# Kernel optimization log

Hardware: AMD Instinct MI355X
Metric: run time of the kernel (lower is better)

## Reference

```python
import jax, jax.numpy as jnp
import numpy as np

NUM_HEADS = 16
FOCUS = 3.0
EPS = 1e-6


def setup_inputs() -> dict:
    key = jax.random.key(0)
    ks = jax.random.split(key, 6)
    B, N, C = 8, 4096, 1024
    x = jax.random.normal(ks[0], (B, N, C), dtype=jnp.float32)
    scale = jax.random.normal(ks[1], (1, 1, C), dtype=jnp.float32) * 0.02
    pos_enc = jax.random.normal(ks[2], (1, N, C), dtype=jnp.float32) * 0.02
    qkv_w = jax.random.normal(ks[3], (3 * C, C), dtype=jnp.float32) * (C ** -0.5)
    proj_w = jax.random.normal(ks[4], (C, C), dtype=jnp.float32) * (C ** -0.5)
    proj_b = jnp.zeros((C,), dtype=jnp.float32)
    return {"x": x, "scale": scale, "pos_enc": pos_enc, "qkv_w": qkv_w,
            "proj_w": proj_w, "proj_b": proj_b}


def reference(x, scale, pos_enc, qkv_w, proj_w, proj_b):
    B, N, C = x.shape
    h = NUM_HEADS
    # qkv projection (no bias)
    qkv = jnp.einsum('bnc,dc->bnd', x, qkv_w).reshape(B, N, 3, C)
    q, k, v = qkv[:, :, 0], qkv[:, :, 1], qkv[:, :, 2]
    k = k + pos_enc
    sc = jax.nn.softplus(scale)  # (1,1,C)
    q = jax.nn.relu(q) + EPS
    k = jax.nn.relu(k) + EPS
    q = q / sc
    k = k / sc
    q_norm = jnp.linalg.norm(q, axis=-1, keepdims=True)
    k_norm = jnp.linalg.norm(k, axis=-1, keepdims=True)
    # focusing_factor = 3 <= 6 branch
    q = q ** FOCUS
    k = k ** FOCUS
    q = q / jnp.linalg.norm(q, axis=-1, keepdims=True) * q_norm
    k = k / jnp.linalg.norm(k, axis=-1, keepdims=True) * k_norm
    # split heads: b n (h c) -> (b h) n c
    def split_heads(t):
        return t.reshape(B, N, h, C // h).transpose(0, 2, 1, 3).reshape(B * h, N, C // h)
    q, k, v = split_heads(q), split_heads(k), split_heads(v)
    q = q.astype(jnp.float32); k = k.astype(jnp.float32); v = v.astype(jnp.float32)
    z = 1.0 / (jnp.einsum('bic,bc->bi', q, k.sum(axis=1)) + EPS)  # (bh, N)
    # kv-first linear attention path (i*j*(c+d) > c*d*(i+j) for these shapes)
    kv = jnp.einsum('bjc,bjd->bcd', k, v)  # (bh, c, d)
    o = jnp.einsum('bic,bcd,bi->bid', q, kv, z)
    # merge heads: (b h) n c -> b n (h c)
    o = o.reshape(B, h, N, C // h).transpose(0, 2, 1, 3).reshape(B, N, C)
    o = jnp.einsum('bnc,dc->bnd', o, proj_w) + proj_b
    return o
```

## Files before the change

### kernel.cpp

```cpp
#include <hip/hip_runtime.h>
#include <hip/hip_bf16.h>
#include <cstdint>
#include <cstddef>


typedef __bf16 bf16;
typedef __bf16 bf16x4 __attribute__((ext_vector_type(4)));
typedef __bf16 bf16x8 __attribute__((ext_vector_type(8)));
typedef float f32x4 __attribute__((ext_vector_type(4)));
typedef float f32x2 __attribute__((ext_vector_type(2)));

#define NB 8
#define NSEQ 4096
#define NC 1024
#define NH 16
#define ND 64
#define NBH 128
#define NM 32768
#define EPSF 1e-6f
#define KSPLIT 8

__device__ __forceinline__ void async16(const void* g, void* l) {
  __builtin_amdgcn_global_load_lds(
      (const __attribute__((address_space(1))) void*)g,
      (__attribute__((address_space(3))) void*)l, 16, 0, 0);
}

__device__ __forceinline__ unsigned pack_bf16(float a, float b) {
  union { bf16 h[2]; unsigned u; } t;
  t.h[0] = (bf16)a; t.h[1] = (bf16)b;
  return t.u;
}

__device__ __forceinline__ unsigned pack2(bf16 a, bf16 b) {
  union { bf16 h[2]; unsigned u; } t;
  t.h[0] = a; t.h[1] = b;
  return t.u;
}

#define BAR() asm volatile("s_barrier" ::: "memory")
#define WAIT_VM(N) asm volatile("s_waitcnt vmcnt(" #N ")" ::: "memory")

__global__ __launch_bounds__(256) void cvt_bf16(const float* __restrict__ src,
                                                bf16* __restrict__ dst, int n4) {
  int i = blockIdx.x * 256 + threadIdx.x;
  if (i < n4) {
    f32x4 v = ((const f32x4*)src)[i];
    bf16x4 o;
    o[0] = (bf16)v[0]; o[1] = (bf16)v[1]; o[2] = (bf16)v[2]; o[3] = (bf16)v[3];
    ((bf16x4*)dst)[i] = o;
  }
}

__global__ __launch_bounds__(256) void prep_scale(const float* __restrict__ scale,
                                                  float* __restrict__ inv_sc) {
  int c = blockIdx.x * 256 + threadIdx.x;
  if (c < NC) inv_sc[c] = 1.0f / log1pf(expf(scale[c]));
}

template <int MODE>
__global__ __launch_bounds__(512, 2) void gemm_bt8(const bf16* __restrict__ A,
                                                   const bf16* __restrict__ Bm, int K,
                                                   bf16* __restrict__ outqk,
                                                   bf16* __restrict__ outv,
                                                   float* __restrict__ outf,
                                                   const float* __restrict__ bias) {
  __shared__ bf16 As[2 * 16384];
  __shared__ bf16 Bs[2 * 16384];

  const int tid = threadIdx.x;
  const int w = tid >> 6, lane = tid & 63;
  const int q4 = lane >> 4, l16 = lane & 15;
  const int l7 = l16 & 7;
  const int wm = (w >> 2) * 128, wn = (w & 3) * 64;

  const int gx = gridDim.x;
  const int nwg = gx * gridDim.y;
  const int bid0 = blockIdx.y * gx + blockIdx.x;
  const int cpx = nwg >> 3;
  const int bid = (bid0 & 7) * cpx + (bid0 >> 3);
  const long row0 = (long)(bid / gx) * 256;
  const long col0 = (long)(bid % gx) * 256;

  const int s0 = w * 128 + lane;
  const int ra = s0 >> 3;
  const int cg = ((s0 & 7) ^ (ra & 7)) << 3;
  const int dl = s0 << 3;

  const bf16* Abase = A + (row0 + ra) * (long)K + cg;
  const bf16* Bbase = Bm + (col0 + ra) * (long)K + cg;
  const long rstep = 8 * (long)K;
  const long hstep = 128 * (long)K;

  auto stA = [&](int buf, int h, int k0) {
    const bf16* g = Abase + h * hstep + k0;
    bf16* l = As + buf * 16384 + h * 8192 + dl;
    async16(g, l);
    async16(g + rstep, l + 512);
  };
  auto stB = [&](int buf, int h, int k0) {
    const bf16* g = Bbase + h * hstep + k0;
    bf16* l = Bs + buf * 16384 + h * 8192 + dl;
    async16(g, l);
    async16(g + rstep, l + 512);
  };

  const int nkt = K >> 6;

  stA(0, 0, 0); stA(0, 1, 0);
  stB(0, 0, 0); stB(0, 1, 0);
  {
    const int k1p = (nkt > 1 ? 1 : 0) << 6;
    stB(1, 0, k1p); stB(1, 1, k1p);
  }
  WAIT_VM(4);
  BAR();

  f32x4 acc[8][4] = {};
  bf16x8 af[4][2], bfr[4][2];

  for (int t = 0; t < nkt; ++t) {
    const int p = t & 1, q = p ^ 1;
    const int pb = p * 16384;
    const int k1 = (t + 1 < nkt ? t + 1 : nkt - 1) << 6;
    const int k2 = (t + 2 < nkt ? t + 2 : nkt - 1) << 6;

#pragma unroll
    for (int mi = 0; mi < 4; mi++) {
      const int rb = (wm + mi * 16 + l16) * 64;
#pragma unroll
      for (int ks = 0; ks < 2; ks++)
        af[mi][ks] = *(const bf16x8*)&As[pb + rb + (((ks * 4 + q4) ^ l7) << 3)];
    }
#pragma unroll
    for (int ni = 0; ni < 2; ni++) {
      const int rb = (wn + ni * 16 + l16) * 64;
#pragma unroll
      for (int ks = 0; ks < 2; ks++)
        bfr[ni][ks] = *(const bf16x8*)&Bs[pb + rb + (((ks * 4 + q4) ^ l7) << 3)];
    }
    stA(q, 0, k1);
    __builtin_amdgcn_s_setprio(1);
#pragma unroll
    for (int mi = 0; mi < 4; mi++)
#pragma unroll
      for (int ni = 0; ni < 2; ni++)
#pragma unroll
        for (int ks = 0; ks < 2; ks++)
          acc[mi][ni] = __builtin_amdgcn_mfma_f32_16x16x32_bf16(
              af[mi][ks], bfr[ni][ks], acc[mi][ni], 0, 0, 0);
    __builtin_amdgcn_s_setprio(0);
    BAR();

#pragma unroll
    for (int ni = 2; ni < 4; ni++) {
      const int rb = (wn + ni * 16 + l16) * 64;
#pragma unroll
      for (int ks = 0; ks < 2; ks++)
        bfr[ni][ks] = *(const bf16x8*)&Bs[pb + rb + (((ks * 4 + q4) ^ l7) << 3)];
    }
    stA(q, 1, k1);
    __builtin_amdgcn_s_setprio(1);
#pragma unroll
    for (int mi = 0; mi < 4; mi++)
#pragma unroll
      for (int ni = 2; ni < 4; ni++)
#pragma unroll
        for (int ks = 0; ks < 2; ks++)
          acc[mi][ni] = __builtin_amdgcn_mfma_f32_16x16x32_bf16(
              af[mi][ks], bfr[ni][ks], acc[mi][ni], 0, 0, 0);
    __builtin_amdgcn_s_setprio(0);
    BAR();

#pragma unroll
    for (int mi = 0; mi < 4; mi++) {
      const int rb = (wm + 64 + mi * 16 + l16) * 64;
#pragma unroll
      for (int ks = 0; ks < 2; ks++)
        af[mi][ks] = *(const bf16x8*)&As[pb + rb + (((ks * 4 + q4) ^ l7) << 3)];
    }
    stB(p, 0, k2);
    __builtin_amdgcn_s_setprio(1);
#pragma unroll
    for (int mi = 0; mi < 4; mi++)
#pragma unroll
      for (int ni = 0; ni < 2; ni++)
#pragma unroll
        for (int ks = 0; ks < 2; ks++)
          acc[4 + mi][ni] = __builtin_amdgcn_mfma_f32_16x16x32_bf16(
              af[mi][ks], bfr[ni][ks], acc[4 + mi][ni], 0, 0, 0);
    __builtin_amdgcn_s_setprio(0);
    BAR();

    stB(p, 1, k2);
    __builtin_amdgcn_s_setprio(1);
#pragma unroll
    for (int mi = 0; mi < 4; mi++)
#pragma unroll
      for (int ni = 2; ni < 4; ni++)
#pragma unroll
        for (int ks = 0; ks < 2; ks++)
          acc[4 + mi][ni] = __builtin_amdgcn_mfma_f32_16x16x32_bf16(
              af[mi][ks], bfr[ni][ks], acc[4 + mi][ni], 0, 0, 0);
    __builtin_amdgcn_s_setprio(0);
    WAIT_VM(4);
    BAR();
  }
  WAIT_VM(0);

  const int ev = (l16 & 1) == 0;
#pragma unroll
  for (int mi = 0; mi < 8; mi++) {
    long gr0 = row0 + wm + mi * 16 + q4 * 4;
#pragma unroll
    for (int ni = 0; ni < 4; ni++) {
      long gc = col0 + wn + ni * 16 + l16;
      long cb = gc & ~1L;
      long r2 = gr0 + (ev ? 0 : 2);
      if (MODE == 0) {
        unsigned m01 = pack_bf16(acc[mi][ni][0], acc[mi][ni][1]);
        unsigned m23 = pack_bf16(acc[mi][ni][2], acc[mi][ni][3]);
        unsigned p01 = __shfl_xor(m01, 1);
        unsigned p23 = __shfl_xor(m23, 1);
        unsigned xs = ev ? m01 : p23;
        unsigned ys = ev ? p01 : m23;
        unsigned da = (xs & 0xFFFFu) | (ys << 16);
        unsigned db = (xs >> 16) | (ys & 0xFFFF0000u);
        if (col0 < 2048) {
          *(unsigned*)(outqk + r2 * 2048 + cb) = da;
          *(unsigned*)(outqk + (r2 + 1) * 2048 + cb) = db;
        } else {
          *(unsigned*)(outv + r2 * 1024 + (cb - 2048)) = da;
          *(unsigned*)(outv + (r2 + 1) * 1024 + (cb - 2048)) = db;
        }
      } else {
        float bsum = bias[gc];
        float v0 = acc[mi][ni][0] + bsum, v1 = acc[mi][ni][1] + bsum;
        float v2 = acc[mi][ni][2] + bsum, v3 = acc[mi][ni][3] + bsum;
        float p0 = __shfl_xor(v0, 1), p1 = __shfl_xor(v1, 1);
        float p2 = __shfl_xor(v2, 1), p3 = __shfl_xor(v3, 1);
        f32x2 sa, sb;
        sa[0] = ev ? v0 : p2; sa[1] = ev ? p0 : v2;
        sb[0] = ev ? v1 : p3; sb[1] = ev ? p1 : v3;
        *(f32x2*)(outf + r2 * 1024 + cb) = sa;
        *(f32x2*)(outf + (r2 + 1) * 1024 + cb) = sb;
      }
    }
  }
}

__global__ __launch_bounds__(256) void transform_qk(const bf16* __restrict__ qkb,
                                                    const bf16* __restrict__ peb,
                                                    const float* __restrict__ inv_sc,
                                                    bf16* __restrict__ qp,
                                                    bf16* __restrict__ kp) {
  const int wave = threadIdx.x >> 6, lane = threadIdx.x & 63;
  const long row = (long)blockIdx.x * 4 + wave;
  const int n = (int)(row & (NSEQ - 1));
  const int c0 = lane * 16;

  bf16x8 qh0 = *(const bf16x8*)(qkb + row * 2048 + c0);
  bf16x8 qh1 = *(const bf16x8*)(qkb + row * 2048 + c0 + 8);
  bf16x8 kh0 = *(const bf16x8*)(qkb + row * 2048 + 1024 + c0);
  bf16x8 kh1 = *(const bf16x8*)(qkb + row * 2048 + 1024 + c0 + 8);
  bf16x8 ph0 = *(const bf16x8*)(peb + (long)n * 1024 + c0);
  bf16x8 ph1 = *(const bf16x8*)(peb + (long)n * 1024 + c0 + 8);
  f32x4 isc[4];
#pragma unroll
  for (int j = 0; j < 4; j++) isc[j] = *(const f32x4*)(inv_sc + c0 + j * 4);

  float q3v[16], k3v[16];
  float s2q = 0.f, s6q = 0.f, s2k = 0.f, s6k = 0.f;
#pragma unroll
  for (int j = 0; j < 16; j++) {
    float qb = (float)(j < 8 ? qh0[j & 7] : qh1[j & 7]);
    float kb = (float)(j < 8 ? kh0[j & 7] : kh1[j & 7]);
    float pe = (float)(j < 8 ? ph0[j & 7] : ph1[j & 7]);
    float is = isc[j >> 2][j & 3];
    float qv = (fmaxf(qb, 0.f) + EPSF) * is;
    float kv = (fmaxf(kb + pe, 0.f) + EPSF) * is;
    float q3 = qv * qv * qv, k3 = kv * kv * kv;
    q3v[j] = q3; k3v[j] = k3;
    s2q += qv * qv; s6q += q3 * q3;
    s2k += kv * kv; s6k += k3 * k3;
  }
#pragma unroll
  for (int off = 32; off > 0; off >>= 1) {
    s2q += __shfl_xor(s2q, off);
    s6q += __shfl_xor(s6q, off);
    s2k += __shfl_xor(s2k, off);
    s6k += __shfl_xor(s6k, off);
  }
  const float fq = sqrtf(s2q / s6q);
  const float fk = sqrtf(s2k / s6k);

  bf16x8 qo0, qo1, ko0, ko1;
#pragma unroll
  for (int j = 0; j < 8; j++) {
    qo0[j] = (bf16)(q3v[j] * fq);     qo1[j] = (bf16)(q3v[8 + j] * fq);
    ko0[j] = (bf16)(k3v[j] * fk);     ko1[j] = (bf16)(k3v[8 + j] * fk);
  }
  *(bf16x8*)(qp + row * 1024 + c0) = qo0;
  *(bf16x8*)(qp + row * 1024 + c0 + 8) = qo1;
  *(bf16x8*)(kp + row * 1024 + c0) = ko0;
  *(bf16x8*)(kp + row * 1024 + c0 + 8) = ko1;
}

__global__ __launch_bounds__(256) void kv_mfma(const bf16* __restrict__ kp,
                                               const bf16* __restrict__ vb,
                                               float* __restrict__ kv_part,
                                               float* __restrict__ ks_part) {
  __shared__ bf16 kT[64 * 64];
  __shared__ bf16 vT[64 * 64];
  const int sp = blockIdx.x;
  const int bh = blockIdx.y;
  const int b = bh >> 4, h = bh & 15;
  const int tid = threadIdx.x;
  const int w = tid >> 6, lane = tid & 63;
  const int q4 = lane >> 4, l16 = lane & 15;
  const int nr = (tid >> 3) * 2;
  const int cg = (tid & 7) * 8;
  const int ng = ((nr >> 3) & 7);

  f32x4 acc[4] = {};
  f32x4 aks = {};
  bf16x8 ones;
#pragma unroll
  for (int j = 0; j < 8; j++) ones[j] = (bf16)1.0f;

  for (int chunk = 0; chunk < NSEQ / KSPLIT / 64; ++chunk) {
    const int n0 = sp * (NSEQ / KSPLIT) + chunk * 64;
    __syncthreads();
    {
      const long g = ((long)(b * NSEQ + n0 + nr)) * NC + h * ND + cg;
      bf16x8 k0 = *(const bf16x8*)(kp + g);
      bf16x8 k1 = *(const bf16x8*)(kp + g + NC);
      bf16x8 v0 = *(const bf16x8*)(vb + g);
      bf16x8 v1 = *(const bf16x8*)(vb + g + NC);
#pragma unroll
      for (int j = 0; j < 8; j++) {
        const int c = cg + j;
        const int idx = c * 64 + ((ng ^ (c & 7)) << 3) + (nr & 7);
        *(unsigned*)&kT[idx] = pack2(k0[j], k1[j]);
        *(unsigned*)&vT[idx] = pack2(v0[j], v1[j]);
      }
    }
    __syncthreads();
#pragma unroll
    for (int kk = 0; kk < 2; kk++) {
      const int cA = w * 16 + l16;
      bf16x8 af = *(const bf16x8*)&kT[cA * 64 + (((kk * 4 + q4) ^ (cA & 7)) << 3)];
#pragma unroll
      for (int dt = 0; dt < 4; dt++) {
        const int dR = dt * 16 + l16;
        bf16x8 bf_ = *(const bf16x8*)&vT[dR * 64 + (((kk * 4 + q4) ^ (dR & 7)) << 3)];
        acc[dt] = __builtin_amdgcn_mfma_f32_16x16x32_bf16(af, bf_, acc[dt], 0, 0, 0);
      }
      aks = __builtin_amdgcn_mfma_f32_16x16x32_bf16(af, ones, aks, 0, 0, 0);
    }
  }
  const long base = ((long)(sp * NBH + bh)) * 4096;
  const int c0 = w * 16 + q4 * 4;
#pragma unroll
  for (int ri = 0; ri < 4; ri++) {
#pragma unroll
    for (int dt = 0; dt < 4; dt++)
      kv_part[base + (long)(c0 + ri) * 64 + dt * 16 + l16] = acc[dt][ri];
  }
  if (l16 == 0) {
#pragma unroll
    for (int ri = 0; ri < 4; ri++)
      ks_part[(long)(sp * NBH + bh) * 64 + c0 + ri] = aks[ri];
  }
}

__global__ __launch_bounds__(256) void reduce_parts(const float* __restrict__ src,
                                                    float* __restrict__ dst, int n) {
  int i = blockIdx.x * 256 + threadIdx.x;
  if (i < n) {
    float s = 0.f;
    for (int p = 0; p < KSPLIT; ++p) s += src[(long)p * n + i];
    dst[i] = s;
  }
}

__global__ __launch_bounds__(256) void z_o(const bf16* __restrict__ qp,
                                           const float* __restrict__ kvm,
                                           const float* __restrict__ ksum,
                                           bf16* __restrict__ ob) {
  __shared__ float kvs[4096];
  __shared__ float kss[64];
  const int bh = blockIdx.x >> 4, chunk = blockIdx.x & 15;
  const int b = bh >> 4, h = bh & 15;
  const int tid = threadIdx.x;
  const int rg = tid >> 2;
  const int qd = (tid & 3) * 16;

  for (int i = tid; i < 1024; i += 256)
    *(f32x4*)&kvs[i * 4] = *(const f32x4*)&kvm[(long)bh * 4096 + i * 4];
  if (tid < 16)
    *(f32x4*)&kss[tid * 4] = *(const f32x4*)&ksum[(long)bh * 64 + tid * 4];
  __syncthreads();

  const long i0 = (long)b * NSEQ + chunk * 256 + rg * 4;
  const bf16* q0 = qp + i0 * NC + h * ND;

  f32x4 o4[4][4] = {};
  float s[4] = {0.f, 0.f, 0.f, 0.f};
  for (int c8 = 0; c8 < 8; ++c8) {
    bf16x8 q8[4];
#pragma unroll
    for (int r = 0; r < 4; r++) q8[r] = *(const bf16x8*)(q0 + r * NC + c8 * 8);
#pragma unroll
    for (int j = 0; j < 8; j++) {
      const int c = c8 * 8 + j;
      const f32x4* kr = (const f32x4*)&kvs[c * 64 + qd];
      const f32x4 k0 = kr[0], k1 = kr[1], k2 = kr[2], k3 = kr[3];
      const float ksc = kss[c];
#pragma unroll
      for (int r = 0; r < 4; r++) {
        const float qc = (float)q8[r][j];
        o4[r][0] += qc * k0; o4[r][1] += qc * k1;
        o4[r][2] += qc * k2; o4[r][3] += qc * k3;
        s[r] += qc * ksc;
      }
    }
  }
#pragma unroll
  for (int r = 0; r < 4; r++) {
    const float z = 1.0f / (s[r] + EPSF);
    bf16* orow = ob + (i0 + r) * NC + h * ND + qd;
#pragma unroll
    for (int d4 = 0; d4 < 4; d4++) {
      bf16x4 o;
#pragma unroll
      for (int j = 0; j < 4; j++) o[j] = (bf16)(o4[r][d4][j] * z);
      *(bf16x4*)(orow + d4 * 4) = o;
    }
  }
}

extern "C" void kernel_launch(void* const* d_in, const int* in_sizes, int n_in,
                              void* d_out, int out_size, void* d_ws, size_t ws_size,
                              hipStream_t stream) {
  const float* x = (const float*)d_in[0];
  const float* scale = (const float*)d_in[1];
  const float* pos_enc = (const float*)d_in[2];
  const float* qkv_w = (const float*)d_in[3];
  const float* proj_w = (const float*)d_in[4];
  const float* proj_b = (const float*)d_in[5];
  float* out = (float*)d_out;

  char* ws = (char*)d_ws;
  size_t off = 0;
  auto alloc = [&](size_t bytes) {
    char* p = ws + off;
    off += (bytes + 255) & ~(size_t)255;
    return p;
  };
  bf16* xb = (bf16*)alloc((size_t)NM * NC * 2);
  bf16* wqkv = (bf16*)alloc((size_t)3 * NC * NC * 2);
  bf16* wproj = (bf16*)alloc((size_t)NC * NC * 2);
  float* inv_sc = (float*)alloc(NC * 4);
  bf16* peb = (bf16*)alloc((size_t)NSEQ * NC * 2);
  bf16* vb = (bf16*)alloc((size_t)NM * NC * 2);
  bf16* kp = (bf16*)alloc((size_t)NM * NC * 2);
  float* ks_part = (float*)alloc((size_t)KSPLIT * NBH * ND * 4);
  float* ksum = (float*)alloc((size_t)NBH * ND * 4);
  float* kvm = (float*)alloc((size_t)NBH * ND * ND * 4);
  bf16* qkb = (bf16*)alloc((size_t)NM * 2048 * 2);
  (void)ws_size; (void)n_in; (void)in_sizes; (void)out_size;

  bf16* ob = (bf16*)qkb;
  float* kv_part = (float*)((char*)qkb + (size_t)NM * NC * 2);
  bf16* qp = xb;

  cvt_bf16<<<dim3((NM * NC / 4 + 255) / 256), 256, 0, stream>>>(x, xb, NM * NC / 4);
  cvt_bf16<<<dim3((3 * NC * NC / 4 + 255) / 256), 256, 0, stream>>>(qkv_w, wqkv, 3 * NC * NC / 4);
  cvt_bf16<<<dim3((NC * NC / 4 + 255) / 256), 256, 0, stream>>>(proj_w, wproj, NC * NC / 4);
  cvt_bf16<<<dim3((NSEQ * NC / 4 + 255) / 256), 256, 0, stream>>>(pos_enc, peb, NSEQ * NC / 4);
  prep_scale<<<dim3(4), 256, 0, stream>>>(scale, inv_sc);

  gemm_bt8<0><<<dim3(12, 128), 512, 0, stream>>>(xb, wqkv, NC, qkb, vb, nullptr, nullptr);

  transform_qk<<<dim3(NM / 4), 256, 0, stream>>>(qkb, peb, inv_sc, qp, kp);

  kv_mfma<<<dim3(KSPLIT, NBH), 256, 0, stream>>>(kp, vb, kv_part, ks_part);
  reduce_parts<<<dim3((NBH * ND + 255) / 256), 256, 0, stream>>>(ks_part, ksum, NBH * ND);
  reduce_parts<<<dim3((NBH * 4096 + 255) / 256), 256, 0, stream>>>(kv_part, kvm, NBH * 4096);

  z_o<<<dim3(NBH * 16), 256, 0, stream>>>(qp, kvm, ksum, ob);

  gemm_bt8<1><<<dim3(4, 128), 512, 0, stream>>>(ob, wproj, NC, nullptr, nullptr, out, proj_b);
}
```

Baseline: 727.4 us.

## Collapse four-phase GEMM k-loop into single load-all then compute phase

Restructures the GEMM main loop from four interleaved phases with barriers into one phase. All A and B fragments for the tile are now loaded from LDS up front, the next A stage is issued, all 64 MFMAs run, and B prefetch follows a single barrier. This removes two barriers per k-step and simplifies scheduling, but raises VGPR pressure (extra ag fragments) and gives up the fine-grained overlap of LDS reads and global prefetch with the MFMAs.

```diff
diff --git a/kernel.cpp b/kernel.cpp
--- a/kernel.cpp
+++ b/kernel.cpp
@@ -117,7 +117,6 @@
   BAR();
 
   f32x4 acc[8][4] = {};
-  bf16x8 af[4][2], bfr[4][2];
 
   for (int t = 0; t < nkt; ++t) {
     const int p = t & 1, q = p ^ 1;
@@ -125,84 +124,48 @@
     const int k1 = (t + 1 < nkt ? t + 1 : nkt - 1) << 6;
     const int k2 = (t + 2 < nkt ? t + 2 : nkt - 1) << 6;
 
+    bf16x8 af[4][2], ag[4][2], bfr[4][2];
 #pragma unroll
     for (int mi = 0; mi < 4; mi++) {
-      const int rb = (wm + mi * 16 + l16) * 64;
-#pragma unroll
-      for (int ks = 0; ks < 2; ks++)
-        af[mi][ks] = *(const bf16x8*)&As[pb + rb + (((ks * 4 + q4) ^ l7) << 3)];
-    }
-#pragma unroll
-    for (int ni = 0; ni < 2; ni++) {
+      const int rb0 = (wm + mi * 16 + l16) * 64;
+      const int rb1 = (wm + 64 + mi * 16 + l16) * 64;
+#pragma unroll
+      for (int ks = 0; ks < 2; ks++) {
+        af[mi][ks] = *(const bf16x8*)&As[pb + rb0 + (((ks * 4 + q4) ^ l7) << 3)];
+        ag[mi][ks] = *(const bf16x8*)&As[pb + rb1 + (((ks * 4 + q4) ^ l7) << 3)];
+      }
+    }
+#pragma unroll
+    for (int ni = 0; ni < 4; ni++) {
       const int rb = (wn + ni * 16 + l16) * 64;
 #pragma unroll
       for (int ks = 0; ks < 2; ks++)
         bfr[ni][ks] = *(const bf16x8*)&Bs[pb + rb + (((ks * 4 + q4) ^ l7) << 3)];
     }
-    stA(q, 0, k1);
+
+    stA(q, 0, k1); stA(q, 1, k1);
+
     __builtin_amdgcn_s_setprio(1);
 #pragma unroll
     for (int mi = 0; mi < 4; mi++)
 #pragma unroll
-      for (int ni = 0; ni < 2; ni++)
+      for (int ni = 0; ni < 4; ni++)
 #pragma unroll
         for (int ks = 0; ks < 2; ks++)
           acc[mi][ni] = __builtin_amdgcn_mfma_f32_16x16x32_bf16(
               af[mi][ks], bfr[ni][ks], acc[mi][ni], 0, 0, 0);
-    __builtin_amdgcn_s_setprio(0);
-    BAR();
-
-#pragma unroll
-    for (int ni = 2; ni < 4; ni++) {
-      const int rb = (wn + ni * 16 + l16) * 64;
-#pragma unroll
-      for (int ks = 0; ks < 2; ks++)
-        bfr[ni][ks] = *(const bf16x8*)&Bs[pb + rb + (((ks * 4 + q4) ^ l7) << 3)];
-    }
-    stA(q, 1, k1);
-    __builtin_amdgcn_s_setprio(1);
 #pragma unroll
     for (int mi = 0; mi < 4; mi++)
 #pragma unroll
-      for (int ni = 2; ni < 4; ni++)
-#pragma unroll
-        for (int ks = 0; ks < 2; ks++)
-          acc[mi][ni] = __builtin_amdgcn_mfma_f32_16x16x32_bf16(
-              af[mi][ks], bfr[ni][ks], acc[mi][ni], 0, 0, 0);
-    __builtin_amdgcn_s_setprio(0);
-    BAR();
-
-#pragma unroll
-    for (int mi = 0; mi < 4; mi++) {
-      const int rb = (wm + 64 + mi * 16 + l16) * 64;
-#pragma unroll
-      for (int ks = 0; ks < 2; ks++)
-        af[mi][ks] = *(const bf16x8*)&As[pb + rb + (((ks * 4 + q4) ^ l7) << 3)];
-    }
-    stB(p, 0, k2);
-    __builtin_amdgcn_s_setprio(1);
-#pragma unroll
-    for (int mi = 0; mi < 4; mi++)
-#pragma unroll
-      for (int ni = 0; ni < 2; ni++)
+      for (int ni = 0; ni < 4; ni++)
 #pragma unroll
         for (int ks = 0; ks < 2; ks++)
           acc[4 + mi][ni] = __builtin_amdgcn_mfma_f32_16x16x32_bf16(
-              af[mi][ks], bfr[ni][ks], acc[4 + mi][ni], 0, 0, 0);
+              ag[mi][ks], bfr[ni][ks], acc[4 + mi][ni], 0, 0, 0);
     __builtin_amdgcn_s_setprio(0);
+
     BAR();
-
-    stB(p, 1, k2);
-    __builtin_amdgcn_s_setprio(1);
-#pragma unroll
-    for (int mi = 0; mi < 4; mi++)
-#pragma unroll
-      for (int ni = 2; ni < 4; ni++)
-#pragma unroll
-        for (int ks = 0; ks < 2; ks++)
-          acc[4 + mi][ni] = __builtin_amdgcn_mfma_f32_16x16x32_bf16(
-              af[mi][ks], bfr[ni][ks], acc[4 + mi][ni], 0, 0, 0);
-    __builtin_amdgcn_s_setprio(0);
+    stB(p, 0, k2); stB(p, 1, k2);
     WAIT_VM(4);
     BAR();
   }
```

Result: faster. 706.6 us (-2.9%).
